# Kernel optimization log

Measured on AMD Instinct MI355X. Metric: run time of the kernel, lower is better.

The kernel has to match this reference:

```python
import jax, jax.numpy as jnp
import numpy as np
import math

B, S, D, H = 4, 2048, 1024, 16
HD = D // H  # head_dim = 64


def setup_inputs() -> dict:
    key = jax.random.key(0)
    ks = jax.random.split(key, 7)
    s = 0.02
    return {
        "q": jax.random.normal(ks[0], (B, S, D), jnp.float32),
        "k": jax.random.normal(ks[1], (B, S, D), jnp.float32),
        "v": jax.random.normal(ks[2], (B, S, D), jnp.float32),
        "wq": jax.random.normal(ks[3], (D, D), jnp.float32) * s,
        "wk": jax.random.normal(ks[4], (D, D), jnp.float32) * s,
        "wv": jax.random.normal(ks[5], (D, D), jnp.float32) * s,
        "wo": jax.random.normal(ks[6], (D, D), jnp.float32) * s,
    }


def reference(q, k, v, wq, wk, wv, wo):
    # Linear (no bias): y = x @ W.T, W is (out, in)
    xq = jnp.einsum('bsd,ed->bse', q, wq).reshape(B, S, H, HD).transpose(0, 2, 1, 3)
    xk = jnp.einsum('bsd,ed->bse', k, wk).reshape(B, S, H, HD).transpose(0, 2, 1, 3)
    xv = jnp.einsum('bsd,ed->bse', v, wv).reshape(B, S, H, HD).transpose(0, 2, 1, 3)
    scores = jnp.einsum('bhqd,bhkd->bhqk', xq, xk) / math.sqrt(HD)  # [B,H,S,S]
    causal = jnp.tril(jnp.ones((S, S), dtype=bool))
    scores = jnp.where(causal[None, None], scores, jnp.float32(-jnp.inf))
    probs = jax.nn.softmax(scores, axis=-1)  # dropout p=0 -> identity
    out = jnp.einsum('bhqk,bhkd->bhqd', probs, xv)  # [B,H,S,HD]
    out = out.transpose(0, 2, 1, 3).reshape(B, S, D)
    return jnp.einsum('bsd,ed->bse', out, wo)
```

## Files before the change

### kernel.cpp

```cpp
#include <hip/hip_runtime.h>

#define SS 2048
#define DD 1024
#define HH 16
#define HD 64
#define MM 8192

typedef unsigned short ushort_t;
typedef __attribute__((ext_vector_type(8))) short short8;
typedef __attribute__((ext_vector_type(4))) float f32x4;
typedef __attribute__((ext_vector_type(4))) unsigned short us4;
typedef __attribute__((ext_vector_type(8))) unsigned short us8;

__device__ __forceinline__ ushort_t f2bf(float f) {
    union { float f; unsigned u; } x; x.f = f;
    unsigned r = x.u + 0x7fffu + ((x.u >> 16) & 1u);
    return (ushort_t)(r >> 16);
}
__device__ __forceinline__ float bf2f(ushort_t h) {
    union { unsigned u; float f; } x; x.u = ((unsigned)h) << 16; return x.f;
}
__device__ __forceinline__ unsigned pack_bf2(float a, float b) {
    union { float f; unsigned u; } x, y; x.f = a; y.f = b;
    return __builtin_amdgcn_perm(y.u, x.u, 0x07060302u);
}

__device__ __forceinline__ void async16(const void* g, void* l) {
    __builtin_amdgcn_global_load_lds(
        (const __attribute__((address_space(1))) unsigned int*)g,
        (__attribute__((address_space(3))) unsigned int*)l, 16, 0, 0);
}

__global__ void cvt_all(const float* __restrict__ q, const float* __restrict__ k,
                        const float* __restrict__ v, const float* __restrict__ wq,
                        const float* __restrict__ wk, const float* __restrict__ wv,
                        const float* __restrict__ wo, ushort_t* __restrict__ qbf,
                        ushort_t* __restrict__ kbf, ushort_t* __restrict__ vbf,
                        ushort_t* __restrict__ wbf) {
    long i = ((long)blockIdx.x * 256 + threadIdx.x) * 8;
    const float* src; ushort_t* dst;
    if (i < (3l << 23)) {
        int s = (int)(i >> 23);
        long off = i & ((1l << 23) - 1);
        src = ((s == 0) ? q : (s == 1) ? k : v) + off;
        dst = ((s == 0) ? qbf : (s == 1) ? kbf : vbf) + off;
    } else {
        long j = i - (3l << 23);
        int s = (int)(j >> 20);
        src = ((s == 0) ? wq : (s == 1) ? wk : (s == 2) ? wv : wo) + (j & 1048575);
        dst = wbf + j;
    }
    float4 f0 = *(const float4*)src;
    float4 f1 = *(const float4*)(src + 4);
    us8 o;
    o[0] = f2bf(f0.x); o[1] = f2bf(f0.y); o[2] = f2bf(f0.z); o[3] = f2bf(f0.w);
    o[4] = f2bf(f1.x); o[5] = f2bf(f1.y); o[6] = f2bf(f1.z); o[7] = f2bf(f1.w);
    *(us8*)dst = o;
}

__device__ __forceinline__ void epi_scatter(f32x4 acc[4][4], int m0, int n0,
                                            int mode, void* Yv) {
    int tid = threadIdx.x;
    int w = tid >> 6, lane = tid & 63;
    int l16 = lane & 15, quad = lane >> 4;
    int wm = (w >> 1) * 64, wn = (w & 1) * 64;
    #pragma unroll
    for (int mt = 0; mt < 4; ++mt) {
        #pragma unroll
        for (int r = 0; r < 4; ++r) {
            int row = m0 + wm + mt * 16 + quad * 4 + r;
            #pragma unroll
            for (int nt = 0; nt < 4; ++nt) {
                int col = n0 + wn + nt * 16 + l16;
                float vf = acc[mt][nt][r];
                if (mode == 2) {
                    ((float*)Yv)[(size_t)row * DD + col] = vf;
                } else {
                    ushort_t vh = f2bf(vf);
                    int b = row >> 11, s = row & 2047;
                    int h = col >> 6,  hd = col & 63;
                    if (mode == 0) {
                        ((ushort_t*)Yv)[(((size_t)b * HH + h) * SS + s) * HD + hd] = vh;
                    } else {
                        int sp = (s & ~63) | (((s & 15) << 2) | ((s >> 4) & 3));
                        ((ushort_t*)Yv)[(((size_t)b * HH + h) * HD + hd) * SS + sp] = vh;
                    }
                }
            }
        }
    }
}

__global__ __launch_bounds__(256) void proj3f(const ushort_t* __restrict__ qbf,
                                              const ushort_t* __restrict__ kbf,
                                              const ushort_t* __restrict__ vbf,
                                              const ushort_t* __restrict__ Wall,
                                              ushort_t* __restrict__ xq,
                                              ushort_t* __restrict__ xk,
                                              ushort_t* __restrict__ xvT) {
    __shared__ __align__(16) ushort_t As[2][128 * 32];
    __shared__ __align__(16) ushort_t Bs[2][128 * 32];
    int tid = threadIdx.x;
    int w = tid >> 6, lane = tid & 63;
    int l16 = lane & 15, quad = lane >> 4;
    int mat   = (int)(blockIdx.x >> 9);
    int inner = (int)(blockIdx.x & 511);
    int m0 = (inner & 63) * 128;
    int n0 = (inner >> 6) * 128;
    const ushort_t* A  = (mat == 0) ? qbf : (mat == 1) ? kbf : vbf;
    const ushort_t* Bw = Wall + ((size_t)mat << 20);
    int wm = (w >> 1) * 64, wn = (w & 1) * 64;

    f32x4 acc[4][4];
    #pragma unroll
    for (int i = 0; i < 4; ++i)
        #pragma unroll
        for (int j = 0; j < 4; ++j) acc[i][j] = (f32x4){0.f, 0.f, 0.f, 0.f};

    int g0 = w * 64 + lane, r0 = g0 >> 2, j0 = ((g0 & 3) ^ (r0 & 3)) * 8;
    int g1 = g0 + 256,      r1 = g1 >> 2, j1 = ((g1 & 3) ^ (r1 & 3)) * 8;
    int swA = (quad ^ (l16 & 3)) * 8;

    async16(A  + (size_t)(m0 + r0) * DD + j0, &As[0][(size_t)(w * 64) * 8]);
    async16(A  + (size_t)(m0 + r1) * DD + j1, &As[0][(size_t)(256 + w * 64) * 8]);
    async16(Bw + (size_t)(n0 + r0) * DD + j0, &Bs[0][(size_t)(w * 64) * 8]);
    async16(Bw + (size_t)(n0 + r1) * DD + j1, &Bs[0][(size_t)(256 + w * 64) * 8]);

    for (int kk = 0; kk < 32; ++kk) {
        int c = kk & 1;
        __syncthreads();
        if (kk < 31) {
            int k1 = (kk + 1) * 32;
            async16(A  + (size_t)(m0 + r0) * DD + k1 + j0, &As[c ^ 1][(size_t)(w * 64) * 8]);
            async16(A  + (size_t)(m0 + r1) * DD + k1 + j1, &As[c ^ 1][(size_t)(256 + w * 64) * 8]);
            async16(Bw + (size_t)(n0 + r0) * DD + k1 + j0, &Bs[c ^ 1][(size_t)(w * 64) * 8]);
            async16(Bw + (size_t)(n0 + r1) * DD + k1 + j1, &Bs[c ^ 1][(size_t)(256 + w * 64) * 8]);
        }
        short8 af[4], bfr[4];
        #pragma unroll
        for (int t = 0; t < 4; ++t) {
            af[t]  = *(const short8*)&As[c][(wm + t * 16 + l16) * 32 + swA];
            bfr[t] = *(const short8*)&Bs[c][(wn + t * 16 + l16) * 32 + swA];
        }
        #pragma unroll
        for (int mt = 0; mt < 4; ++mt)
            #pragma unroll
            for (int nt = 0; nt < 4; ++nt)
                acc[mt][nt] = __builtin_amdgcn_mfma_f32_16x16x32_bf16(af[mt], bfr[nt], acc[mt][nt], 0, 0, 0);
    }

    void* Y = (mat == 0) ? (void*)xq : (mat == 1) ? (void*)xk : (void*)xvT;
    epi_scatter(acc, m0, n0, (mat == 2) ? 1 : 0, Y);
}

__global__ __launch_bounds__(256) void out_gemm(const ushort_t* __restrict__ Abf,
                                                const ushort_t* __restrict__ Bw,
                                                float* __restrict__ Y) {
    __shared__ __align__(16) ushort_t As[2][128 * 32];
    __shared__ __align__(16) ushort_t Bs[2][128 * 32];
    int tid = threadIdx.x;
    int w = tid >> 6, lane = tid & 63;
    int l16 = lane & 15, quad = lane >> 4;
    int m0 = (int)(blockIdx.x & 63) * 128;
    int n0 = (int)(blockIdx.x >> 6) * 128;
    int wm = (w >> 1) * 64, wn = (w & 1) * 64;

    f32x4 acc[4][4];
    #pragma unroll
    for (int i = 0; i < 4; ++i)
        #pragma unroll
        for (int j = 0; j < 4; ++j) acc[i][j] = (f32x4){0.f, 0.f, 0.f, 0.f};

    int g0 = w * 64 + lane, r0 = g0 >> 2, j0 = ((g0 & 3) ^ (r0 & 3)) * 8;
    int g1 = g0 + 256,      r1 = g1 >> 2, j1 = ((g1 & 3) ^ (r1 & 3)) * 8;
    int swA = (quad ^ (l16 & 3)) * 8;

    async16(Abf + (size_t)(m0 + r0) * DD + j0, &As[0][(size_t)(w * 64) * 8]);
    async16(Abf + (size_t)(m0 + r1) * DD + j1, &As[0][(size_t)(256 + w * 64) * 8]);
    async16(Bw  + (size_t)(n0 + r0) * DD + j0, &Bs[0][(size_t)(w * 64) * 8]);
    async16(Bw  + (size_t)(n0 + r1) * DD + j1, &Bs[0][(size_t)(256 + w * 64) * 8]);

    for (int kk = 0; kk < 32; ++kk) {
        int c = kk & 1;
        __syncthreads();
        if (kk < 31) {
            int k1 = (kk + 1) * 32;
            async16(Abf + (size_t)(m0 + r0) * DD + k1 + j0, &As[c ^ 1][(size_t)(w * 64) * 8]);
            async16(Abf + (size_t)(m0 + r1) * DD + k1 + j1, &As[c ^ 1][(size_t)(256 + w * 64) * 8]);
            async16(Bw  + (size_t)(n0 + r0) * DD + k1 + j0, &Bs[c ^ 1][(size_t)(w * 64) * 8]);
            async16(Bw  + (size_t)(n0 + r1) * DD + k1 + j1, &Bs[c ^ 1][(size_t)(256 + w * 64) * 8]);
        }
        short8 af[4], bfr[4];
        #pragma unroll
        for (int t = 0; t < 4; ++t) {
            af[t]  = *(const short8*)&As[c][(wm + t * 16 + l16) * 32 + swA];
            bfr[t] = *(const short8*)&Bs[c][(wn + t * 16 + l16) * 32 + swA];
        }
        #pragma unroll
        for (int mt = 0; mt < 4; ++mt)
            #pragma unroll
            for (int nt = 0; nt < 4; ++nt)
                acc[mt][nt] = __builtin_amdgcn_mfma_f32_16x16x32_bf16(af[mt], bfr[nt], acc[mt][nt], 0, 0, 0);
    }
    epi_scatter(acc, m0, n0, 2, Y);
}

__global__ __launch_bounds__(256) void attn_kernel(const ushort_t* __restrict__ xq,
                                                   const ushort_t* __restrict__ xk,
                                                   const ushort_t* __restrict__ xvT,
                                                   ushort_t* __restrict__ ao) {
    __shared__ __align__(16) ushort_t Ksm[2][64 * 64];
    __shared__ __align__(16) ushort_t Vsm[2][64 * 64];
    __shared__ __align__(16) ushort_t Psm[4][16 * 72];

    int tid = threadIdx.x;
    int w = tid >> 6, lane = tid & 63;
    int l16 = lane & 15, quad = lane >> 4;
    int bh = blockIdx.x & 63;
    int p  = blockIdx.x >> 6;
    int b = bh >> 4, h = bh & 15;

    const ushort_t* Q  = xq  + (size_t)bh * SS * HD;
    const ushort_t* K  = xk  + (size_t)bh * SS * HD;
    const ushort_t* VT = xvT + (size_t)bh * HD * SS;

    int g0 = w * 64 + lane, r0 = g0 >> 3, j0 = ((g0 & 7) ^ (r0 & 7)) * 8;
    int g1 = g0 + 256,      r1 = g1 >> 3, j1 = ((g1 & 7) ^ (r1 & 7)) * 8;

    short8 ones;
    #pragma unroll
    for (int i = 0; i < 8; ++i) ones[i] = (short)0x3F80;

    const float CS = 0.125f * 1.44269504f;

    for (int ph = 0; ph < 2; ++ph) {
        int qt = ph ? (31 - p) : p;
        int qb = qt * 64;
        int qmin = qb + w * 16;

        short8 aq[2];
        #pragma unroll
        for (int kc = 0; kc < 2; ++kc) {
            short8 t = *(const short8*)(Q + (size_t)(qmin + l16) * HD + kc * 32 + quad * 8);
            #pragma unroll
            for (int i = 0; i < 8; ++i)
                t[i] = (short)f2bf(bf2f((ushort_t)t[i]) * CS);
            aq[kc] = t;
        }

        f32x4 o[4];
        #pragma unroll
        for (int dt = 0; dt < 4; ++dt) o[dt] = (f32x4){0.f, 0.f, 0.f, 0.f};
        f32x4 lacc = (f32x4){0.f, 0.f, 0.f, 0.f};

        __syncthreads();
        async16(K  + (size_t)r0 * HD + j0, &Ksm[0][(size_t)(w * 64) * 8]);
        async16(K  + (size_t)r1 * HD + j1, &Ksm[0][(size_t)(256 + w * 64) * 8]);
        async16(VT + (size_t)r0 * SS + j0, &Vsm[0][(size_t)(w * 64) * 8]);
        async16(VT + (size_t)r1 * SS + j1, &Vsm[0][(size_t)(256 + w * 64) * 8]);

        for (int kt = 0; kt <= qt; ++kt) {
            int kb = kt * 64;
            int c = kt & 1;
            __syncthreads();
            if (kt < qt) {
                int kb1 = kb + 64;
                async16(K  + (size_t)(kb1 + r0) * HD + j0, &Ksm[c ^ 1][(size_t)(w * 64) * 8]);
                async16(K  + (size_t)(kb1 + r1) * HD + j1, &Ksm[c ^ 1][(size_t)(256 + w * 64) * 8]);
                async16(VT + (size_t)r0 * SS + kb1 + j0, &Vsm[c ^ 1][(size_t)(w * 64) * 8]);
                async16(VT + (size_t)r1 * SS + kb1 + j1, &Vsm[c ^ 1][(size_t)(256 + w * 64) * 8]);
            }

            f32x4 sc[4];
            #pragma unroll
            for (int nt = 0; nt < 4; ++nt) {
                int row = nt * 16 + l16;
                short8 bk0 = *(const short8*)&Ksm[c][row * 64 + ((0 + quad) ^ (l16 & 7)) * 8];
                short8 bk1 = *(const short8*)&Ksm[c][row * 64 + ((4 + quad) ^ (l16 & 7)) * 8];
                f32x4 cc = (f32x4){0.f, 0.f, 0.f, 0.f};
                cc = __builtin_amdgcn_mfma_f32_16x16x32_bf16(aq[0], bk0, cc, 0, 0, 0);
                cc = __builtin_amdgcn_mfma_f32_16x16x32_bf16(aq[1], bk1, cc, 0, 0, 0);
                sc[nt] = cc;
            }

            bool msk = (kt == qt);
            #pragma unroll
            for (int r = 0; r < 4; ++r) {
                float e0, e1, e2, e3;
                if (msk) {
                    int qg = qmin + quad * 4 + r;
                    e0 = (kb +  0 + l16 <= qg) ? __builtin_amdgcn_exp2f(sc[0][r]) : 0.f;
                    e1 = (kb + 16 + l16 <= qg) ? __builtin_amdgcn_exp2f(sc[1][r]) : 0.f;
                    e2 = (kb + 32 + l16 <= qg) ? __builtin_amdgcn_exp2f(sc[2][r]) : 0.f;
                    e3 = (kb + 48 + l16 <= qg) ? __builtin_amdgcn_exp2f(sc[3][r]) : 0.f;
                } else {
                    e0 = __builtin_amdgcn_exp2f(sc[0][r]);
                    e1 = __builtin_amdgcn_exp2f(sc[1][r]);
                    e2 = __builtin_amdgcn_exp2f(sc[2][r]);
                    e3 = __builtin_amdgcn_exp2f(sc[3][r]);
                }
                uint2 pk = { pack_bf2(e0, e1), pack_bf2(e2, e3) };
                *(uint2*)&Psm[w][(quad * 4 + r) * 72 + l16 * 4] = pk;
            }

            asm volatile("s_waitcnt lgkmcnt(0)" ::: "memory");

            #pragma unroll
            for (int kc = 0; kc < 2; ++kc) {
                short8 ap = *(const short8*)&Psm[w][l16 * 72 + kc * 32 + quad * 8];
                lacc = __builtin_amdgcn_mfma_f32_16x16x32_bf16(ap, ones, lacc, 0, 0, 0);
                #pragma unroll
                for (int dt = 0; dt < 4; ++dt) {
                    int row = dt * 16 + l16;
                    short8 bv = *(const short8*)&Vsm[c][row * 64 + ((kc * 4 + quad) ^ (l16 & 7)) * 8];
                    o[dt] = __builtin_amdgcn_mfma_f32_16x16x32_bf16(ap, bv, o[dt], 0, 0, 0);
                }
            }
        }

        #pragma unroll
        for (int r = 0; r < 4; ++r) {
            float inv = 1.0f / lacc[r];
            int qg = qmin + quad * 4 + r;
            #pragma unroll
            for (int dt = 0; dt < 4; ++dt)
                ao[((size_t)(b * SS + qg)) * DD + h * HD + dt * 16 + l16] = f2bf(o[dt][r] * inv);
        }
    }
}

extern "C" void kernel_launch(void* const* d_in, const int* in_sizes, int n_in,
                              void* d_out, int out_size, void* d_ws, size_t ws_size,
                              hipStream_t stream) {
    const float* q  = (const float*)d_in[0];
    const float* k  = (const float*)d_in[1];
    const float* v  = (const float*)d_in[2];
    const float* wq = (const float*)d_in[3];
    const float* wk = (const float*)d_in[4];
    const float* wv = (const float*)d_in[5];
    const float* wo = (const float*)d_in[6];
    float* out = (float*)d_out;

    ushort_t* wbf = (ushort_t*)d_ws;
    ushort_t* xq  = wbf + 4194304ull;
    ushort_t* xk  = xq  + 8388608ull;
    ushort_t* xvT = xk  + 8388608ull;
    ushort_t* ao  = xvT + 8388608ull;
    ushort_t* vbf = ao;
    ushort_t* qbf = (ushort_t*)d_out;
    ushort_t* kbf = qbf + 8388608ull;

    cvt_all<<<14336, 256, 0, stream>>>(q, k, v, wq, wk, wv, wo, qbf, kbf, vbf, wbf);
    proj3f<<<1536, 256, 0, stream>>>(qbf, kbf, vbf, wbf, xq, xk, xvT);
    attn_kernel<<<1024, 256, 0, stream>>>(xq, xk, xvT, ao);
    out_gemm<<<512, 256, 0, stream>>>(ao, wbf + 3145728ull, out);
}
```

Before: 342.7 us.

## Use 256x128 GEMM tiles with 512-thread blocks and MFMA priority hints in attention

Both projection GEMMs now use 512-thread blocks computing 256x128 output tiles. This shares each staged weight (B) tile across twice as many rows and halves the block count. The attention kernel wraps its MFMA sections in s_setprio raises, so waves issuing matrix ops are favoured over waves doing softmax and exp. The larger tiles mean fewer blocks (768 and 256), which could underfill the CUs for out_gemm and adds LDS per block.

```diff
diff --git a/kernel.cpp b/kernel.cpp
--- a/kernel.cpp
+++ b/kernel.cpp
@@ -58,20 +58,18 @@
     *(us8*)dst = o;
 }
 
-__device__ __forceinline__ void epi_scatter(f32x4 acc[4][4], int m0, int n0,
+__device__ __forceinline__ void epi_scatter(f32x4 acc[4][4], int bm, int bn,
                                             int mode, void* Yv) {
-    int tid = threadIdx.x;
-    int w = tid >> 6, lane = tid & 63;
+    int lane = threadIdx.x & 63;
     int l16 = lane & 15, quad = lane >> 4;
-    int wm = (w >> 1) * 64, wn = (w & 1) * 64;
     #pragma unroll
     for (int mt = 0; mt < 4; ++mt) {
         #pragma unroll
         for (int r = 0; r < 4; ++r) {
-            int row = m0 + wm + mt * 16 + quad * 4 + r;
+            int row = bm + mt * 16 + quad * 4 + r;
             #pragma unroll
             for (int nt = 0; nt < 4; ++nt) {
-                int col = n0 + wn + nt * 16 + l16;
+                int col = bn + nt * 16 + l16;
                 float vf = acc[mt][nt][r];
                 if (mode == 2) {
                     ((float*)Yv)[(size_t)row * DD + col] = vf;
@@ -91,22 +89,22 @@
     }
 }
 
-__global__ __launch_bounds__(256) void proj3f(const ushort_t* __restrict__ qbf,
+__global__ __launch_bounds__(512) void proj3f(const ushort_t* __restrict__ qbf,
                                               const ushort_t* __restrict__ kbf,
                                               const ushort_t* __restrict__ vbf,
                                               const ushort_t* __restrict__ Wall,
                                               ushort_t* __restrict__ xq,
                                               ushort_t* __restrict__ xk,
                                               ushort_t* __restrict__ xvT) {
-    __shared__ __align__(16) ushort_t As[2][128 * 32];
+    __shared__ __align__(16) ushort_t As[2][256 * 32];
     __shared__ __align__(16) ushort_t Bs[2][128 * 32];
     int tid = threadIdx.x;
     int w = tid >> 6, lane = tid & 63;
     int l16 = lane & 15, quad = lane >> 4;
-    int mat   = (int)(blockIdx.x >> 9);
-    int inner = (int)(blockIdx.x & 511);
-    int m0 = (inner & 63) * 128;
-    int n0 = (inner >> 6) * 128;
+    int mat   = (int)(blockIdx.x >> 8);
+    int inner = (int)(blockIdx.x & 255);
+    int m0 = (inner & 31) * 256;
+    int n0 = (inner >> 5) * 128;
     const ushort_t* A  = (mat == 0) ? qbf : (mat == 1) ? kbf : vbf;
     const ushort_t* Bw = Wall + ((size_t)mat << 20);
     int wm = (w >> 1) * 64, wn = (w & 1) * 64;
@@ -117,24 +115,24 @@
         #pragma unroll
         for (int j = 0; j < 4; ++j) acc[i][j] = (f32x4){0.f, 0.f, 0.f, 0.f};
 
-    int g0 = w * 64 + lane, r0 = g0 >> 2, j0 = ((g0 & 3) ^ (r0 & 3)) * 8;
-    int g1 = g0 + 256,      r1 = g1 >> 2, j1 = ((g1 & 3) ^ (r1 & 3)) * 8;
+    int ra0 = tid >> 2,           ja0 = ((tid & 3) ^ (ra0 & 3)) * 8;
+    int ga1 = tid + 512;
+    int ra1 = ga1 >> 2,           ja1 = ((ga1 & 3) ^ (ra1 & 3)) * 8;
+    int rb  = tid >> 2,           jb  = ((tid & 3) ^ (rb & 3)) * 8;
     int swA = (quad ^ (l16 & 3)) * 8;
 
-    async16(A  + (size_t)(m0 + r0) * DD + j0, &As[0][(size_t)(w * 64) * 8]);
-    async16(A  + (size_t)(m0 + r1) * DD + j1, &As[0][(size_t)(256 + w * 64) * 8]);
-    async16(Bw + (size_t)(n0 + r0) * DD + j0, &Bs[0][(size_t)(w * 64) * 8]);
-    async16(Bw + (size_t)(n0 + r1) * DD + j1, &Bs[0][(size_t)(256 + w * 64) * 8]);
+    async16(A  + (size_t)(m0 + ra0) * DD + ja0, &As[0][(size_t)(w * 64) * 8]);
+    async16(A  + (size_t)(m0 + ra1) * DD + ja1, &As[0][(size_t)(512 + w * 64) * 8]);
+    async16(Bw + (size_t)(n0 + rb)  * DD + jb,  &Bs[0][(size_t)(w * 64) * 8]);
 
     for (int kk = 0; kk < 32; ++kk) {
         int c = kk & 1;
         __syncthreads();
         if (kk < 31) {
             int k1 = (kk + 1) * 32;
-            async16(A  + (size_t)(m0 + r0) * DD + k1 + j0, &As[c ^ 1][(size_t)(w * 64) * 8]);
-            async16(A  + (size_t)(m0 + r1) * DD + k1 + j1, &As[c ^ 1][(size_t)(256 + w * 64) * 8]);
-            async16(Bw + (size_t)(n0 + r0) * DD + k1 + j0, &Bs[c ^ 1][(size_t)(w * 64) * 8]);
-            async16(Bw + (size_t)(n0 + r1) * DD + k1 + j1, &Bs[c ^ 1][(size_t)(256 + w * 64) * 8]);
+            async16(A  + (size_t)(m0 + ra0) * DD + k1 + ja0, &As[c ^ 1][(size_t)(w * 64) * 8]);
+            async16(A  + (size_t)(m0 + ra1) * DD + k1 + ja1, &As[c ^ 1][(size_t)(512 + w * 64) * 8]);
+            async16(Bw + (size_t)(n0 + rb)  * DD + k1 + jb,  &Bs[c ^ 1][(size_t)(w * 64) * 8]);
         }
         short8 af[4], bfr[4];
         #pragma unroll
@@ -150,19 +148,20 @@
     }
 
     void* Y = (mat == 0) ? (void*)xq : (mat == 1) ? (void*)xk : (void*)xvT;
-    epi_scatter(acc, m0, n0, (mat == 2) ? 1 : 0, Y);
-}
-
-__global__ __launch_bounds__(256) void out_gemm(const ushort_t* __restrict__ Abf,
+    epi_scatter(acc, m0 + wm, n0 + wn, (mat == 2) ? 1 : 0, Y);
+}
+
+__global__ __launch_bounds__(512) void out_gemm(const ushort_t* __restrict__ Abf,
                                                 const ushort_t* __restrict__ Bw,
                                                 float* __restrict__ Y) {
-    __shared__ __align__(16) ushort_t As[2][128 * 32];
+    __shared__ __align__(16) ushort_t As[2][256 * 32];
     __shared__ __align__(16) ushort_t Bs[2][128 * 32];
     int tid = threadIdx.x;
     int w = tid >> 6, lane = tid & 63;
     int l16 = lane & 15, quad = lane >> 4;
-    int m0 = (int)(blockIdx.x & 63) * 128;
-    int n0 = (int)(blockIdx.x >> 6) * 128;
+    int inner = (int)blockIdx.x;
+    int m0 = (inner & 31) * 256;
+    int n0 = (inner >> 5) * 128;
     int wm = (w >> 1) * 64, wn = (w & 1) * 64;
 
     f32x4 acc[4][4];
@@ -171,24 +170,24 @@
         #pragma unroll
         for (int j = 0; j < 4; ++j) acc[i][j] = (f32x4){0.f, 0.f, 0.f, 0.f};
 
-    int g0 = w * 64 + lane, r0 = g0 >> 2, j0 = ((g0 & 3) ^ (r0 & 3)) * 8;
-    int g1 = g0 + 256,      r1 = g1 >> 2, j1 = ((g1 & 3) ^ (r1 & 3)) * 8;
+    int ra0 = tid >> 2,           ja0 = ((tid & 3) ^ (ra0 & 3)) * 8;
+    int ga1 = tid + 512;
+    int ra1 = ga1 >> 2,           ja1 = ((ga1 & 3) ^ (ra1 & 3)) * 8;
+    int rb  = tid >> 2,           jb  = ((tid & 3) ^ (rb & 3)) * 8;
     int swA = (quad ^ (l16 & 3)) * 8;
 
-    async16(Abf + (size_t)(m0 + r0) * DD + j0, &As[0][(size_t)(w * 64) * 8]);
-    async16(Abf + (size_t)(m0 + r1) * DD + j1, &As[0][(size_t)(256 + w * 64) * 8]);
-    async16(Bw  + (size_t)(n0 + r0) * DD + j0, &Bs[0][(size_t)(w * 64) * 8]);
-    async16(Bw  + (size_t)(n0 + r1) * DD + j1, &Bs[0][(size_t)(256 + w * 64) * 8]);
+    async16(Abf + (size_t)(m0 + ra0) * DD + ja0, &As[0][(size_t)(w * 64) * 8]);
+    async16(Abf + (size_t)(m0 + ra1) * DD + ja1, &As[0][(size_t)(512 + w * 64) * 8]);
+    async16(Bw  + (size_t)(n0 + rb)  * DD + jb,  &Bs[0][(size_t)(w * 64) * 8]);
 
     for (int kk = 0; kk < 32; ++kk) {
         int c = kk & 1;
         __syncthreads();
         if (kk < 31) {
             int k1 = (kk + 1) * 32;
-            async16(Abf + (size_t)(m0 + r0) * DD + k1 + j0, &As[c ^ 1][(size_t)(w * 64) * 8]);
-            async16(Abf + (size_t)(m0 + r1) * DD + k1 + j1, &As[c ^ 1][(size_t)(256 + w * 64) * 8]);
-            async16(Bw  + (size_t)(n0 + r0) * DD + k1 + j0, &Bs[c ^ 1][(size_t)(w * 64) * 8]);
-            async16(Bw  + (size_t)(n0 + r1) * DD + k1 + j1, &Bs[c ^ 1][(size_t)(256 + w * 64) * 8]);
+            async16(Abf + (size_t)(m0 + ra0) * DD + k1 + ja0, &As[c ^ 1][(size_t)(w * 64) * 8]);
+            async16(Abf + (size_t)(m0 + ra1) * DD + k1 + ja1, &As[c ^ 1][(size_t)(512 + w * 64) * 8]);
+            async16(Bw  + (size_t)(n0 + rb)  * DD + k1 + jb,  &Bs[c ^ 1][(size_t)(w * 64) * 8]);
         }
         short8 af[4], bfr[4];
         #pragma unroll
@@ -202,7 +201,7 @@
             for (int nt = 0; nt < 4; ++nt)
                 acc[mt][nt] = __builtin_amdgcn_mfma_f32_16x16x32_bf16(af[mt], bfr[nt], acc[mt][nt], 0, 0, 0);
     }
-    epi_scatter(acc, m0, n0, 2, Y);
+    epi_scatter(acc, m0 + wm, n0 + wn, 2, Y);
 }
 
 __global__ __launch_bounds__(256) void attn_kernel(const ushort_t* __restrict__ xq,
@@ -272,6 +271,7 @@
             }
 
             f32x4 sc[4];
+            __builtin_amdgcn_s_setprio(1);
             #pragma unroll
             for (int nt = 0; nt < 4; ++nt) {
                 int row = nt * 16 + l16;
@@ -282,6 +282,7 @@
                 cc = __builtin_amdgcn_mfma_f32_16x16x32_bf16(aq[1], bk1, cc, 0, 0, 0);
                 sc[nt] = cc;
             }
+            __builtin_amdgcn_s_setprio(0);
 
             bool msk = (kt == qt);
             #pragma unroll
@@ -305,6 +306,7 @@
 
             asm volatile("s_waitcnt lgkmcnt(0)" ::: "memory");
 
+            __builtin_amdgcn_s_setprio(1);
             #pragma unroll
             for (int kc = 0; kc < 2; ++kc) {
                 short8 ap = *(const short8*)&Psm[w][l16 * 72 + kc * 32 + quad * 8];
@@ -316,6 +318,7 @@
                     o[dt] = __builtin_amdgcn_mfma_f32_16x16x32_bf16(ap, bv, o[dt], 0, 0, 0);
                 }
             }
+            __builtin_amdgcn_s_setprio(0);
         }
 
         #pragma unroll
@@ -351,7 +354,7 @@
     ushort_t* kbf = qbf + 8388608ull;
 
     cvt_all<<<14336, 256, 0, stream>>>(q, k, v, wq, wk, wv, wo, qbf, kbf, vbf, wbf);
-    proj3f<<<1536, 256, 0, stream>>>(qbf, kbf, vbf, wbf, xq, xk, xvT);
+    proj3f<<<768, 512, 0, stream>>>(qbf, kbf, vbf, wbf, xq, xk, xvT);
     attn_kernel<<<1024, 256, 0, stream>>>(xq, xk, xvT, ao);
-    out_gemm<<<512, 256, 0, stream>>>(ao, wbf + 3145728ull, out);
-}
+    out_gemm<<<256, 512, 0, stream>>>(ao, wbf + 3145728ull, out);
+}
```

Result: faster. 333.8 us (-2.6%).
